# Performance work log

Hardware: AMD Instinct MI355X
Metric: run time of the kernel (lower is better)

Reference implementation:

```python
import jax, jax.numpy as jnp
import numpy as np

R = 3                    # correlation radius -> K = (2R+1)^2 = 49
B, C, H, W = 2, 256, 64, 64


def bilinear_sampler(img, coords):
    """RAFT-style bilinear sampler with zero padding, align_corners=True.
    img: [B,C,H,W]; coords: [B,Hp,Wp,2] in pixel space (x, y).
    Returns [B,C,Hp,Wp]."""
    b, c, h, w = img.shape
    x = coords[..., 0]
    y = coords[..., 1]
    x0 = jnp.floor(x)
    y0 = jnp.floor(y)
    x1 = x0 + 1.0
    y1 = y0 + 1.0
    # bilinear corner weights
    w00 = (x1 - x) * (y1 - y)
    w01 = (x - x0) * (y1 - y)
    w10 = (x1 - x) * (y - y0)
    w11 = (x - x0) * (y - y0)
    imgf = img.reshape(b, c, h * w)
    hp, wp = coords.shape[1], coords.shape[2]
    n = hp * wp

    def corner(xi, yi, wt):
        xi = xi.astype(jnp.int32)
        yi = yi.astype(jnp.int32)
        valid = (xi >= 0) & (xi < w) & (yi >= 0) & (yi < h)
        xi_c = jnp.clip(xi, 0, w - 1)
        yi_c = jnp.clip(yi, 0, h - 1)
        idx = (yi_c * w + xi_c).reshape(b, 1, n)            # [B,1,N]
        vals = jnp.take_along_axis(imgf, jnp.broadcast_to(idx, (b, c, n)), axis=2)
        wt = (wt * valid.astype(wt.dtype)).reshape(b, 1, n)  # zero-padding mask
        return vals * wt

    out = (corner(x0, y0, w00) + corner(x1, y0, w01)
           + corner(x0, y1, w10) + corner(x1, y1, w11))
    return out.reshape(b, c, hp, wp)


def setup_inputs() -> dict:
    key = jax.random.key(0)
    k1, k2, k3 = jax.random.split(key, 3)
    f1 = jax.random.normal(k1, (B, C, H, W), dtype=jnp.float32)
    f2 = jax.random.normal(k2, (B, C, H, W), dtype=jnp.float32)
    ys, xs = jnp.meshgrid(jnp.arange(H, dtype=jnp.float32),
                          jnp.arange(W, dtype=jnp.float32), indexing='ij')
    base = jnp.broadcast_to(jnp.stack([xs, ys])[None], (B, 2, H, W))  # identity coords
    c0 = base
    c1 = base + 2.0 * jax.random.normal(k3, (B, 2, H, W), dtype=jnp.float32)  # coords + flow
    return {"f1": f1, "f2": f2, "c1": c1, "c0": c0}


def reference(f1, f2, c1, c0):
    r = R
    b, c, h, w = f1.shape
    # warp f2 by c1
    f2w = bilinear_sampler(f2, jnp.transpose(c1, (0, 2, 3, 1)))
    # window offsets: torch.meshgrid(dy, dx) then stack (dx, dy)
    d = jnp.linspace(-r, r, 2 * r + 1)
    dyg, dxg = jnp.meshgrid(d, d, indexing='ij')
    delta = jnp.stack([dxg, dyg], axis=-1).reshape(-1, 2)   # [K,2]
    grid = c0.reshape(b, 2, h * w).transpose(0, 2, 1)[:, :, None, :]  # [b,hw,1,2]
    x = grid + delta[None, None]                             # [b,hw,K,2]
    win = bilinear_sampler(f2w, x)                           # [b,c,hw,K]
    q = f1.reshape(b, c, h * w)                              # [b,c,hw]
    corr = jnp.einsum('bcn,bcnk->bnk', q, win) / jnp.sqrt(jnp.float32(c))
    corr = corr.reshape(b, h, w, (2 * r + 1) ** 2).transpose(0, 3, 1, 2)  # [b,K,h,w]
    return (c1, corr)
```

## Files before the change

kernel.cpp:

```cpp
#include <hip/hip_runtime.h>
#include <hip/hip_fp16.h>

#define BATCH 2
#define CCH   256
#define WDIM  64
#define HW    4096
#define KWIN  49

#define UW    15
#define UH    11
#define UPOS  165
#define DSTR  177
#define BITEMS (UPOS * 16)
#define NSLOT 6

using f16x8 = __attribute__((ext_vector_type(8))) _Float16;
using f32x4 = __attribute__((ext_vector_type(4))) float;

__device__ __forceinline__ __half2 u2h2(unsigned u) {
    union { unsigned u; __half2 h; } v; v.u = u; return v.h;
}
__device__ __forceinline__ unsigned h22u(__half2 h) {
    union { unsigned u; __half2 h; } v; v.h = h; return v.u;
}
__device__ __forceinline__ f16x8 ldfrag(const ushort* p) {
    return __builtin_bit_cast(f16x8, *(const uint4*)p);
}
__device__ __forceinline__ void blend8(uint4 u, float w, float* a) {
    float2 m;
    m = __half22float2(u2h2(u.x)); a[0] += w * m.x; a[1] += w * m.y;
    m = __half22float2(u2h2(u.y)); a[2] += w * m.x; a[3] += w * m.y;
    m = __half22float2(u2h2(u.z)); a[4] += w * m.x; a[5] += w * m.y;
    m = __half22float2(u2h2(u.w)); a[6] += w * m.x; a[7] += w * m.y;
}
__device__ __forceinline__ uint4 pack8(const float* a) {
    uint4 o;
    o.x = h22u(__float22half2_rn(make_float2(a[0], a[1])));
    o.y = h22u(__float22half2_rn(make_float2(a[2], a[3])));
    o.z = h22u(__float22half2_rn(make_float2(a[4], a[5])));
    o.w = h22u(__float22half2_rn(make_float2(a[6], a[7])));
    return o;
}

__global__ __launch_bounds__(256) void transpose_kernel(
    const float* __restrict__ f1, const float* __restrict__ f2,
    const float* __restrict__ c1, __half* __restrict__ f1t,
    __half* __restrict__ f2t, float* __restrict__ out0)
{
    __shared__ float s1[32][65];
    __shared__ float s2[32][65];

    const int t  = threadIdx.x;
    const int b  = blockIdx.x >> 6;
    const int nb = (blockIdx.x & 63) << 6;
    const int cc = blockIdx.y << 5;

    if (blockIdx.y == 0 && t < 128) {
        const int idx = blockIdx.x * 128 + t;
        out0[idx] = c1[idx];
    }

    const int pix = t & 63;
    const int tq  = t >> 6;
    const int n   = nb + pix;

    const float* f2b = f2 + ((size_t)b * CCH + cc) * HW;
    const float* f1b = f1 + ((size_t)b * CCH + cc) * HW;

    #pragma unroll
    for (int j = 0; j < 8; ++j) {
        const int cl = tq * 8 + j;
        s2[cl][pix] = f2b[(size_t)cl * HW + n];
        s1[cl][pix] = f1b[(size_t)cl * HW + n];
    }
    __syncthreads();

    const int lo = t & 7;
    const int pq = t >> 3;
    ushort* o1 = (ushort*)f1t;
    ushort* o2 = (ushort*)f2t;
    #pragma unroll
    for (int j = 0; j < 2; ++j) {
        const int pix2 = j * 32 + pq;
        const int c4 = 4 * lo;
        const size_t base = ((size_t)(b * HW + nb + pix2)) * CCH + cc + c4;
        uint2 va, vb;
        va.x = h22u(__float22half2_rn(make_float2(s1[c4 + 0][pix2], s1[c4 + 1][pix2])));
        va.y = h22u(__float22half2_rn(make_float2(s1[c4 + 2][pix2], s1[c4 + 3][pix2])));
        vb.x = h22u(__float22half2_rn(make_float2(s2[c4 + 0][pix2], s2[c4 + 1][pix2])));
        vb.y = h22u(__float22half2_rn(make_float2(s2[c4 + 2][pix2], s2[c4 + 3][pix2])));
        *(uint2*)(o1 + base) = va;
        *(uint2*)(o2 + base) = vb;
    }
}

__global__ __launch_bounds__(512) void corr_fused_kernel(
    const __half* __restrict__ f1t, const __half* __restrict__ f2t,
    const float* __restrict__ c1, const float* __restrict__ c0,
    float* __restrict__ outc)
{
    __shared__ __align__(16) char RAW[16384 + 176 * 128 * 2];
    __shared__ float s_fx[32], s_fy[32];
    __shared__ int   s_lbx[32], s_lby[32];
    __shared__ float4 s_cw[UPOS];
    __shared__ int4   s_co[UPOS];

    ushort* A16 = (ushort*)RAW;
    ushort* B16 = (ushort*)(RAW + 16384);
    float*  Dex = (float*)(RAW + 16384);

    const int t  = threadIdx.x;
    const int l  = t & 63;
    const int wv = t >> 6;

    const int bid = blockIdx.x;
    const int swz = (bid & 7) * 32 + (bid >> 3);
    const int b   = swz >> 7;
    const int tau = swz & 127;
    const int ty  = tau >> 3, tx = tau & 7;
    const int n0  = ty * 256 + tx * 8;

    const ushort* f1u = (const ushort*)f1t + ((size_t)b * HW) * CCH;
    const ushort* f2u = (const ushort*)f2t + ((size_t)b * HW) * CCH;

    const int r0 = t >> 5,         c0i = t & 31;
    const int r1 = (t + 512) >> 5, c1i = (t + 512) & 31;
    const int an0 = n0 + ((r0 >> 3) << 6) + (r0 & 7);
    const int an1 = n0 + ((r1 >> 3) << 6) + (r1 & 7);
    const uint4 av0 = *(const uint4*)(f1u + (size_t)an0 * CCH + c0i * 8);
    const uint4 av1 = *(const uint4*)(f1u + (size_t)an1 * CCH + c1i * 8);

    float pcx = 0.f, pcy = 0.f;
    int ifx = 0, ify = 0;
    if (l < 32) {
        const int n = n0 + ((l >> 3) << 6) + (l & 7);
        pcx = c0[(b * 2 + 0) * HW + n];
        pcy = c0[(b * 2 + 1) * HW + n];
        ifx = (int)floorf(pcx);
        ify = (int)floorf(pcy);
    }
    int mnx = (l < 32) ? ifx : 0x7fffffff;
    int mxx = (l < 32) ? ifx : (-0x7fffffff - 1);
    int mny = (l < 32) ? ify : 0x7fffffff;
    int mxy = (l < 32) ? ify : (-0x7fffffff - 1);
    #pragma unroll
    for (int off = 1; off < 64; off <<= 1) {
        mnx = min(mnx, __shfl_xor(mnx, off, 64));
        mxx = max(mxx, __shfl_xor(mxx, off, 64));
        mny = min(mny, __shfl_xor(mny, off, 64));
        mxy = max(mxy, __shfl_xor(mxy, off, 64));
    }
    const int bx0 = mnx - 3, by0 = mny - 3;
    const int contained = (mxx - mnx <= 7) && (mxy - mny <= 3);

    if (wv == 0 && l < 32) {
        s_fx[l]  = pcx - floorf(pcx);
        s_fy[l]  = pcy - floorf(pcy);
        s_lbx[l] = ifx - mnx;
        s_lby[l] = ify - mny;
    }

    if (t < UPOS) {
        const int wy = t / UW, wx = t - wy * UW;
        const int py = by0 + wy, px = bx0 + wx;
        float4 cw = {0.f, 0.f, 0.f, 0.f};
        int4   co = {0, 0, 0, 0};
        if (px >= 0 && px < WDIM && py >= 0 && py < WDIM) {
            const int np = py * WDIM + px;
            const float cx = c1[(b * 2 + 0) * HW + np];
            const float cy = c1[(b * 2 + 1) * HW + np];
            const float x0f = floorf(cx), y0f = floorf(cy);
            const float fx = cx - x0f, fy = cy - y0f;
            const int ix0 = (int)x0f, iy0 = (int)y0f;
            const int ix1 = ix0 + 1,  iy1 = iy0 + 1;
            float w00 = (1.f - fx) * (1.f - fy);
            float w01 = fx * (1.f - fy);
            float w10 = (1.f - fx) * fy;
            float w11 = fx * fy;
            if (ix0 < 0 || ix0 >= WDIM) { w00 = 0.f; w10 = 0.f; }
            if (ix1 < 0 || ix1 >= WDIM) { w01 = 0.f; w11 = 0.f; }
            if (iy0 < 0 || iy0 >= WDIM) { w00 = 0.f; w01 = 0.f; }
            if (iy1 < 0 || iy1 >= WDIM) { w10 = 0.f; w11 = 0.f; }
            const int xc0 = min(max(ix0, 0), WDIM - 1);
            const int xc1 = min(max(ix1, 0), WDIM - 1);
            const int yc0 = min(max(iy0, 0), WDIM - 1);
            const int yc1 = min(max(iy1, 0), WDIM - 1);
            cw = float4{w00, w01, w10, w11};
            co = int4{yc0 * WDIM + xc0, yc0 * WDIM + xc1,
                      yc1 * WDIM + xc0, yc1 * WDIM + xc1};
        }
        s_cw[t] = cw;
        s_co[t] = co;
    }
    __syncthreads();

    if (contained) {
        uint4 b1r[NSLOT];
        int   bofs[NSLOT];
        #pragma unroll
        for (int k = 0; k < NSLOT; ++k) {
            const int idx = t + k * 512;
            bofs[k] = -1;
            b1r[k] = uint4{0u, 0u, 0u, 0u};
            uint4 h0 = uint4{0u, 0u, 0u, 0u};
            if (idx < BITEMS) {
                const int r = idx >> 4, c = idx & 15;
                bofs[k] = r * 128 + ((c ^ (r & 7)) << 3);
                const float4 cw = s_cw[r];
                const int4   co = s_co[r];
                const ushort* base = f2u + c * 8;
                float a0[8] = {0.f,0.f,0.f,0.f,0.f,0.f,0.f,0.f};
                float a1[8] = {0.f,0.f,0.f,0.f,0.f,0.f,0.f,0.f};
                const ushort* p0 = base + (size_t)co.x * CCH;
                const ushort* p1 = base + (size_t)co.y * CCH;
                const ushort* p2 = base + (size_t)co.z * CCH;
                const ushort* p3 = base + (size_t)co.w * CCH;
                blend8(*(const uint4*)(p0),       cw.x, a0);
                blend8(*(const uint4*)(p0 + 128), cw.x, a1);
                blend8(*(const uint4*)(p1),       cw.y, a0);
                blend8(*(const uint4*)(p1 + 128), cw.y, a1);
                blend8(*(const uint4*)(p2),       cw.z, a0);
                blend8(*(const uint4*)(p2 + 128), cw.z, a1);
                blend8(*(const uint4*)(p3),       cw.w, a0);
                blend8(*(const uint4*)(p3 + 128), cw.w, a1);
                h0 = pack8(a0);
                b1r[k] = pack8(a1);
            }
            if (bofs[k] >= 0) *(uint4*)(B16 + bofs[k]) = h0;
        }

        *(uint4*)(A16 + r0 * 256 + ((c0i ^ (r0 & 7)) << 3)) = av0;
        *(uint4*)(A16 + r1 * 256 + ((c1i ^ (r1 & 7)) << 3)) = av1;
        __syncthreads();

        const int mt = wv & 1;
        const int ng = wv >> 1;
        const int nnt = (ng == 3) ? 2 : 3;
        int nt[3] = {ng, ng + 4, ng + 8};
        f32x4 acc[3];
        #pragma unroll
        for (int i = 0; i < 3; ++i) acc[i] = f32x4{0.f, 0.f, 0.f, 0.f};

        const int g    = l >> 4;
        const int arow = mt * 16 + (l & 15);
        const int axr  = arow & 7;

        {
            f16x8 af[4];
            #pragma unroll
            for (int s = 0; s < 4; ++s)
                af[s] = ldfrag(A16 + arow * 256 + (((s * 4 + g) ^ axr) << 3));
            #pragma unroll
            for (int i = 0; i < 3; ++i) if (i < nnt) {
                const int brow = nt[i] * 16 + (l & 15);
                const int bxr  = brow & 7;
                #pragma unroll
                for (int s = 0; s < 4; ++s) {
                    const f16x8 bf = ldfrag(B16 + brow * 128 + (((s * 4 + g) ^ bxr) << 3));
                    acc[i] = __builtin_amdgcn_mfma_f32_16x16x32_f16(af[s], bf, acc[i], 0, 0, 0);
                }
            }
        }
        __syncthreads();

        #pragma unroll
        for (int k = 0; k < NSLOT; ++k)
            if (bofs[k] >= 0) *(uint4*)(B16 + bofs[k]) = b1r[k];
        __syncthreads();

        {
            f16x8 af[4];
            #pragma unroll
            for (int s = 0; s < 4; ++s)
                af[s] = ldfrag(A16 + arow * 256 + (((16 + s * 4 + g) ^ axr) << 3));
            #pragma unroll
            for (int i = 0; i < 3; ++i) if (i < nnt) {
                const int brow = nt[i] * 16 + (l & 15);
                const int bxr  = brow & 7;
                #pragma unroll
                for (int s = 0; s < 4; ++s) {
                    const f16x8 bf = ldfrag(B16 + brow * 128 + (((s * 4 + g) ^ bxr) << 3));
                    acc[i] = __builtin_amdgcn_mfma_f32_16x16x32_f16(af[s], bf, acc[i], 0, 0, 0);
                }
            }
        }
        __syncthreads();

        #pragma unroll
        for (int i = 0; i < 3; ++i) if (i < nnt) {
            #pragma unroll
            for (int r4 = 0; r4 < 4; ++r4) {
                Dex[(mt * 16 + (l >> 4) * 4 + r4) * DSTR + nt[i] * 16 + (l & 15)] = acc[i][r4];
            }
        }
        __syncthreads();

        for (int idx = t; idx < 32 * KWIN; idx += 512) {
            const int p = idx & 31, k = idx >> 5;
            const int dyi = k / 7, dxi = k - dyi * 7;
            const int pos = (s_lby[p] + dyi) * UW + s_lbx[p] + dxi;
            const float* dr = Dex + p * DSTR + pos;
            const float d00 = dr[0], d01 = dr[1], d10 = dr[UW], d11 = dr[UW + 1];
            const float fx = s_fx[p], fy = s_fy[p];
            const float w00 = (1.f - fx) * (1.f - fy);
            const float w01 = fx * (1.f - fy);
            const float w10 = (1.f - fx) * fy;
            const float w11 = fx * fy;
            const float r = (w00 * d00 + w01 * d01 + w10 * d10 + w11 * d11) * 0.0625f;
            const int n = n0 + ((p >> 3) << 6) + (p & 7);
            outc[(size_t)(b * KWIN + k) * HW + n] = r;
        }
    } else {
        float* sDw = (float*)RAW + wv * 64;
        for (int p = wv; p < 32; p += 8) {
            const int n = n0 + ((p >> 3) << 6) + (p & 7);
            const float cx = c0[(b * 2 + 0) * HW + n];
            const float cy = c0[(b * 2 + 1) * HW + n];
            const float x0f = floorf(cx), y0f = floorf(cy);
            const float fx = cx - x0f, fy = cy - y0f;
            const int bx = (int)x0f - 3, by = (int)y0f - 3;
            const int ix = l & 7, iy = l >> 3;
            const int px = bx + ix, py = by + iy;
            float a = 0.f;
            if (px >= 0 && px < WDIM && py >= 0 && py < WDIM) {
                const int np = py * WDIM + px;
                const float wcx = c1[(b * 2 + 0) * HW + np];
                const float wcy = c1[(b * 2 + 1) * HW + np];
                const float wx0f = floorf(wcx), wy0f = floorf(wcy);
                const float gx = wcx - wx0f, gy = wcy - wy0f;
                const int jx0 = (int)wx0f, jy0 = (int)wy0f;
                const int jx1 = jx0 + 1,   jy1 = jy0 + 1;
                float w00 = (1.f - gx) * (1.f - gy);
                float w01 = gx * (1.f - gy);
                float w10 = (1.f - gx) * gy;
                float w11 = gx * gy;
                if (jx0 < 0 || jx0 >= WDIM) { w00 = 0.f; w10 = 0.f; }
                if (jx1 < 0 || jx1 >= WDIM) { w01 = 0.f; w11 = 0.f; }
                if (jy0 < 0 || jy0 >= WDIM) { w00 = 0.f; w01 = 0.f; }
                if (jy1 < 0 || jy1 >= WDIM) { w10 = 0.f; w11 = 0.f; }
                const int kx0 = min(max(jx0, 0), WDIM - 1);
                const int kx1 = min(max(jx1, 0), WDIM - 1);
                const int ky0 = min(max(jy0, 0), WDIM - 1);
                const int ky1 = min(max(jy1, 0), WDIM - 1);
                const ushort* qr = f1u + (size_t)n * CCH;
                const ushort* e0 = f2u + (size_t)(ky0 * WDIM + kx0) * CCH;
                const ushort* e1 = f2u + (size_t)(ky0 * WDIM + kx1) * CCH;
                const ushort* e2 = f2u + (size_t)(ky1 * WDIM + kx0) * CCH;
                const ushort* e3 = f2u + (size_t)(ky1 * WDIM + kx1) * CCH;
                for (int c = 0; c < 32; ++c) {
                    float w8[8] = {0.f,0.f,0.f,0.f,0.f,0.f,0.f,0.f};
                    blend8(*(const uint4*)(e0 + c * 8), w00, w8);
                    blend8(*(const uint4*)(e1 + c * 8), w01, w8);
                    blend8(*(const uint4*)(e2 + c * 8), w10, w8);
                    blend8(*(const uint4*)(e3 + c * 8), w11, w8);
                    const uint4 uq = *(const uint4*)(qr + c * 8);
                    float q8[8] = {0.f,0.f,0.f,0.f,0.f,0.f,0.f,0.f};
                    blend8(uq, 1.f, q8);
                    #pragma unroll
                    for (int e = 0; e < 8; ++e) a += q8[e] * w8[e];
                }
            }
            sDw[l] = a;
            const int k = l;
            if (k < KWIN) {
                const int dyi = k / 7, dxi = k - dyi * 7;
                const int s = dyi * 8 + dxi;
                const float d00 = sDw[s], d01 = sDw[s + 1];
                const float d10 = sDw[s + 8], d11 = sDw[s + 9];
                const float w00 = (1.f - fx) * (1.f - fy);
                const float w01 = fx * (1.f - fy);
                const float w10 = (1.f - fx) * fy;
                const float w11 = fx * fy;
                const float r = (w00 * d00 + w01 * d01 + w10 * d10 + w11 * d11) * 0.0625f;
                outc[(size_t)(b * KWIN + k) * HW + n] = r;
            }
        }
    }
}

extern "C" void kernel_launch(void* const* d_in, const int* in_sizes, int n_in,
                              void* d_out, int out_size, void* d_ws, size_t ws_size,
                              hipStream_t stream) {
    (void)in_sizes; (void)n_in; (void)out_size; (void)ws_size;
    const float* f1 = (const float*)d_in[0];
    const float* f2 = (const float*)d_in[1];
    const float* c1 = (const float*)d_in[2];
    const float* c0 = (const float*)d_in[3];
    float* out = (float*)d_out;

    const size_t PLANE = (size_t)BATCH * HW * CCH;
    __half* f1t = (__half*)d_ws;
    __half* f2t = f1t + PLANE;

    dim3 g1(BATCH * (HW / 64), CCH / 32);
    transpose_kernel<<<g1, 256, 0, stream>>>(f1, f2, c1, f1t, f2t, out);

    corr_fused_kernel<<<(BATCH * HW) / 32, 512, 0, stream>>>(
        f1t, f2t, c1, c0, out + BATCH * 2 * HW);
}
```

Measured before the change: 20.01 us.

## Double-buffer B tiles, software-pipeline gathers, and blend in packed half2

The shared-memory B buffer is doubled so both channel halves of the warped f2 window are staged at once. This removes the second half's register holding and two block barriers, and lets a single MFMA loop cover all 256 channels. The gather loop is software-pipelined: loads for the next slot are issued before the current slot is blended. The bilinear blend now runs as packed half2 FMAs instead of fp32 accumulation. The cost is more LDS per block (which may reduce occupancy), more live registers, and lower blend precision in fp16.

```diff
diff --git a/kernel.cpp b/kernel.cpp
--- a/kernel.cpp
+++ b/kernel.cpp
@@ -13,6 +13,7 @@
 #define DSTR  177
 #define BITEMS (UPOS * 16)
 #define NSLOT 6
+#define BBYTES (176 * 128 * 2)
 
 using f16x8 = __attribute__((ext_vector_type(8))) _Float16;
 using f32x4 = __attribute__((ext_vector_type(4))) float;
@@ -33,13 +34,14 @@
     m = __half22float2(u2h2(u.z)); a[4] += w * m.x; a[5] += w * m.y;
     m = __half22float2(u2h2(u.w)); a[6] += w * m.x; a[7] += w * m.y;
 }
-__device__ __forceinline__ uint4 pack8(const float* a) {
-    uint4 o;
-    o.x = h22u(__float22half2_rn(make_float2(a[0], a[1])));
-    o.y = h22u(__float22half2_rn(make_float2(a[2], a[3])));
-    o.z = h22u(__float22half2_rn(make_float2(a[4], a[5])));
-    o.w = h22u(__float22half2_rn(make_float2(a[6], a[7])));
-    return o;
+__device__ __forceinline__ unsigned h2fma4(unsigned a, unsigned b, unsigned c,
+                                           unsigned d, __half2 w0, __half2 w1,
+                                           __half2 w2, __half2 w3) {
+    __half2 acc = __hmul2(w0, u2h2(a));
+    acc = __hfma2(w1, u2h2(b), acc);
+    acc = __hfma2(w2, u2h2(c), acc);
+    acc = __hfma2(w3, u2h2(d), acc);
+    return h22u(acc);
 }
 
 __global__ __launch_bounds__(256) void transpose_kernel(
@@ -99,14 +101,15 @@
     const float* __restrict__ c1, const float* __restrict__ c0,
     float* __restrict__ outc)
 {
-    __shared__ __align__(16) char RAW[16384 + 176 * 128 * 2];
+    __shared__ __align__(16) char RAW[16384 + 2 * BBYTES];
     __shared__ float s_fx[32], s_fy[32];
     __shared__ int   s_lbx[32], s_lby[32];
     __shared__ float4 s_cw[UPOS];
     __shared__ int4   s_co[UPOS];
 
     ushort* A16 = (ushort*)RAW;
-    ushort* B16 = (ushort*)(RAW + 16384);
+    ushort* B0  = (ushort*)(RAW + 16384);
+    ushort* B1  = (ushort*)(RAW + 16384 + BBYTES);
     float*  Dex = (float*)(RAW + 16384);
 
     const int t  = threadIdx.x;
@@ -192,45 +195,62 @@
         s_cw[t] = cw;
         s_co[t] = co;
     }
+
+    *(uint4*)(A16 + r0 * 256 + ((c0i ^ (r0 & 7)) << 3)) = av0;
+    *(uint4*)(A16 + r1 * 256 + ((c1i ^ (r1 & 7)) << 3)) = av1;
+
     __syncthreads();
 
     if (contained) {
-        uint4 b1r[NSLOT];
-        int   bofs[NSLOT];
-        #pragma unroll
-        for (int k = 0; k < NSLOT; ++k) {
+        uint4   v0[2][4], v1[2][4];
+        __half2 wb[2][4];
+        int     ob[2];
+
+        auto issueSlot = [&](int k, int buf) {
             const int idx = t + k * 512;
-            bofs[k] = -1;
-            b1r[k] = uint4{0u, 0u, 0u, 0u};
-            uint4 h0 = uint4{0u, 0u, 0u, 0u};
+            ob[buf] = -1;
             if (idx < BITEMS) {
                 const int r = idx >> 4, c = idx & 15;
-                bofs[k] = r * 128 + ((c ^ (r & 7)) << 3);
+                ob[buf] = r * 128 + ((c ^ (r & 7)) << 3);
                 const float4 cw = s_cw[r];
                 const int4   co = s_co[r];
+                wb[buf][0] = __float2half2_rn(cw.x);
+                wb[buf][1] = __float2half2_rn(cw.y);
+                wb[buf][2] = __float2half2_rn(cw.z);
+                wb[buf][3] = __float2half2_rn(cw.w);
                 const ushort* base = f2u + c * 8;
-                float a0[8] = {0.f,0.f,0.f,0.f,0.f,0.f,0.f,0.f};
-                float a1[8] = {0.f,0.f,0.f,0.f,0.f,0.f,0.f,0.f};
                 const ushort* p0 = base + (size_t)co.x * CCH;
                 const ushort* p1 = base + (size_t)co.y * CCH;
                 const ushort* p2 = base + (size_t)co.z * CCH;
                 const ushort* p3 = base + (size_t)co.w * CCH;
-                blend8(*(const uint4*)(p0),       cw.x, a0);
-                blend8(*(const uint4*)(p0 + 128), cw.x, a1);
-                blend8(*(const uint4*)(p1),       cw.y, a0);
-                blend8(*(const uint4*)(p1 + 128), cw.y, a1);
-                blend8(*(const uint4*)(p2),       cw.z, a0);
-                blend8(*(const uint4*)(p2 + 128), cw.z, a1);
-                blend8(*(const uint4*)(p3),       cw.w, a0);
-                blend8(*(const uint4*)(p3 + 128), cw.w, a1);
-                h0 = pack8(a0);
-                b1r[k] = pack8(a1);
-            }
-            if (bofs[k] >= 0) *(uint4*)(B16 + bofs[k]) = h0;
-        }
-
-        *(uint4*)(A16 + r0 * 256 + ((c0i ^ (r0 & 7)) << 3)) = av0;
-        *(uint4*)(A16 + r1 * 256 + ((c1i ^ (r1 & 7)) << 3)) = av1;
+                v0[buf][0] = *(const uint4*)p0;  v1[buf][0] = *(const uint4*)(p0 + 128);
+                v0[buf][1] = *(const uint4*)p1;  v1[buf][1] = *(const uint4*)(p1 + 128);
+                v0[buf][2] = *(const uint4*)p2;  v1[buf][2] = *(const uint4*)(p2 + 128);
+                v0[buf][3] = *(const uint4*)p3;  v1[buf][3] = *(const uint4*)(p3 + 128);
+            }
+        };
+
+        issueSlot(0, 0);
+        #pragma unroll
+        for (int k = 0; k < NSLOT; ++k) {
+            const int cb = k & 1;
+            if (k + 1 < NSLOT) issueSlot(k + 1, cb ^ 1);
+            if (ob[cb] >= 0) {
+                const __half2 w0 = wb[cb][0], w1 = wb[cb][1];
+                const __half2 w2 = wb[cb][2], w3 = wb[cb][3];
+                uint4 o0, o1;
+                o0.x = h2fma4(v0[cb][0].x, v0[cb][1].x, v0[cb][2].x, v0[cb][3].x, w0, w1, w2, w3);
+                o0.y = h2fma4(v0[cb][0].y, v0[cb][1].y, v0[cb][2].y, v0[cb][3].y, w0, w1, w2, w3);
+                o0.z = h2fma4(v0[cb][0].z, v0[cb][1].z, v0[cb][2].z, v0[cb][3].z, w0, w1, w2, w3);
+                o0.w = h2fma4(v0[cb][0].w, v0[cb][1].w, v0[cb][2].w, v0[cb][3].w, w0, w1, w2, w3);
+                o1.x = h2fma4(v1[cb][0].x, v1[cb][1].x, v1[cb][2].x, v1[cb][3].x, w0, w1, w2, w3);
+                o1.y = h2fma4(v1[cb][0].y, v1[cb][1].y, v1[cb][2].y, v1[cb][3].y, w0, w1, w2, w3);
+                o1.z = h2fma4(v1[cb][0].z, v1[cb][1].z, v1[cb][2].z, v1[cb][3].z, w0, w1, w2, w3);
+                o1.w = h2fma4(v1[cb][0].w, v1[cb][1].w, v1[cb][2].w, v1[cb][3].w, w0, w1, w2, w3);
+                *(uint4*)(B0 + ob[cb]) = o0;
+                *(uint4*)(B1 + ob[cb]) = o1;
+            }
+        }
         __syncthreads();
 
         const int mt = wv & 1;
@@ -246,41 +266,22 @@
         const int axr  = arow & 7;
 
         {
-            f16x8 af[4];
+            f16x8 af[8];
             #pragma unroll
-            for (int s = 0; s < 4; ++s)
-                af[s] = ldfrag(A16 + arow * 256 + (((s * 4 + g) ^ axr) << 3));
+            for (int s = 0; s < 4; ++s) {
+                af[s]     = ldfrag(A16 + arow * 256 + (((s * 4 + g) ^ axr) << 3));
+                af[4 + s] = ldfrag(A16 + arow * 256 + (((16 + s * 4 + g) ^ axr) << 3));
+            }
             #pragma unroll
             for (int i = 0; i < 3; ++i) if (i < nnt) {
                 const int brow = nt[i] * 16 + (l & 15);
                 const int bxr  = brow & 7;
                 #pragma unroll
                 for (int s = 0; s < 4; ++s) {
-                    const f16x8 bf = ldfrag(B16 + brow * 128 + (((s * 4 + g) ^ bxr) << 3));
-                    acc[i] = __builtin_amdgcn_mfma_f32_16x16x32_f16(af[s], bf, acc[i], 0, 0, 0);
-                }
-            }
-        }
-        __syncthreads();
-
-        #pragma unroll
-        for (int k = 0; k < NSLOT; ++k)
-            if (bofs[k] >= 0) *(uint4*)(B16 + bofs[k]) = b1r[k];
-        __syncthreads();
-
-        {
-            f16x8 af[4];
-            #pragma unroll
-            for (int s = 0; s < 4; ++s)
-                af[s] = ldfrag(A16 + arow * 256 + (((16 + s * 4 + g) ^ axr) << 3));
-            #pragma unroll
-            for (int i = 0; i < 3; ++i) if (i < nnt) {
-                const int brow = nt[i] * 16 + (l & 15);
-                const int bxr  = brow & 7;
-                #pragma unroll
-                for (int s = 0; s < 4; ++s) {
-                    const f16x8 bf = ldfrag(B16 + brow * 128 + (((s * 4 + g) ^ bxr) << 3));
-                    acc[i] = __builtin_amdgcn_mfma_f32_16x16x32_f16(af[s], bf, acc[i], 0, 0, 0);
+                    const f16x8 bf0 = ldfrag(B0 + brow * 128 + (((s * 4 + g) ^ bxr) << 3));
+                    acc[i] = __builtin_amdgcn_mfma_f32_16x16x32_f16(af[s], bf0, acc[i], 0, 0, 0);
+                    const f16x8 bf1 = ldfrag(B1 + brow * 128 + (((s * 4 + g) ^ bxr) << 3));
+                    acc[i] = __builtin_amdgcn_mfma_f32_16x16x32_f16(af[4 + s], bf1, acc[i], 0, 0, 0);
                 }
             }
         }
```

Result: faster. 19.02 us (-5.0%).
